# Kernel tuning notes

Hardware: AMD Instinct MI355X
Metric: run time of the kernel (lower is better)

## Reference

```python
import jax, jax.numpy as jnp
import numpy as np

D_MODEL, D_QK, D_V = 1024, 128, 128
B, S = 4, 4096


def setup_inputs() -> dict:
    key = jax.random.key(0)
    ks = jax.random.split(key, 4)
    scale = 1.0 / np.sqrt(D_MODEL)
    return {
        "x": jax.random.normal(ks[0], (B, S, D_MODEL), dtype=jnp.float32),
        "Wq": jax.random.normal(ks[1], (D_MODEL, D_QK), dtype=jnp.float32) * scale,
        "bq": jnp.zeros((D_QK,), dtype=jnp.float32),
        "Wk": jax.random.normal(ks[2], (D_MODEL, D_QK), dtype=jnp.float32) * scale,
        "bk": jnp.zeros((D_QK,), dtype=jnp.float32),
        "Wv": jax.random.normal(ks[3], (D_MODEL, D_V), dtype=jnp.float32) * scale,
        "bv": jnp.zeros((D_V,), dtype=jnp.float32),
    }


def reference(x, Wq, bq, Wk, bk, Wv, bv):
    # Linear projections (torch Linear: x @ W^T + b; here W stored as [in, out])
    q = jnp.einsum("bsd,de->bse", x, Wq) + bq  # [B, S, d_qk]
    k = jnp.einsum("bsd,de->bse", x, Wk) + bk  # [B, S, d_qk]
    v = jnp.einsum("bsd,de->bse", x, Wv) + bv  # [B, S, d_v]
    scores = jnp.einsum("bqe,bke->bqk", q, k) / jnp.sqrt(jnp.float32(D_QK))
    attn = jax.nn.softmax(scores, axis=-1)  # [B, S, S]
    return jnp.einsum("bqk,bkv->bqv", attn, v)  # [B, S, d_v]
```

## Files before the change

kernel.cpp:

```cpp
#include <hip/hip_runtime.h>
#include <math.h>

#define DM    1024
#define DQK   128
#define BATCH 4
#define SEQ   4096
#define QSCALE (0.08838834764831845f * 1.4426950408889634f)
#define DEFER_THR 6.0f

typedef _Float16 f16;
typedef _Float16 f16x4 __attribute__((ext_vector_type(4)));
typedef _Float16 f16x8 __attribute__((ext_vector_type(8)));
typedef float    f32x4 __attribute__((ext_vector_type(4)));

__global__ __launch_bounds__(256) void wcvt_kernel(
    const float* __restrict__ Wq, const float* __restrict__ bq,
    const float* __restrict__ Wk, const float* __restrict__ bk,
    const float* __restrict__ Wv, const float* __restrict__ bv,
    f16* __restrict__ wt, float* __restrict__ biasf)
{
    const int sel = blockIdx.x >> 3;
    const int k0  = (blockIdx.x & 7) * 128;
    const float* W; const float* b; float sc;
    if (sel == 0)      { W = Wq; b = bq; sc = QSCALE; }
    else if (sel == 1) { W = Wk; b = bk; sc = 1.0f; }
    else               { W = Wv; b = bv; sc = 1.0f; }

    __shared__ f16 tile[128][136];

    #pragma unroll
    for (int it = 0; it < 16; ++it) {
        int flat = threadIdx.x + it * 256;
        int kk   = flat >> 5;
        int c4   = flat & 31;
        float4 w4 = *(const float4*)(W + (size_t)(k0 + kk) * DQK + c4 * 4);
        tile[kk][c4 * 4 + 0] = (f16)(w4.x * sc);
        tile[kk][c4 * 4 + 1] = (f16)(w4.y * sc);
        tile[kk][c4 * 4 + 2] = (f16)(w4.z * sc);
        tile[kk][c4 * 4 + 3] = (f16)(w4.w * sc);
    }
    __syncthreads();

    #pragma unroll
    for (int it = 0; it < 8; ++it) {
        int flat = threadIdx.x + it * 256;
        int n    = flat >> 4;
        int kc   = flat & 15;
        f16x8 v;
        #pragma unroll
        for (int i = 0; i < 8; ++i) v[i] = tile[kc * 8 + i][n];
        *(f16x8*)(wt + (size_t)(sel * 128 + n) * DM + k0 + kc * 8) = v;
    }
    if ((blockIdx.x & 7) == 0 && threadIdx.x < 128)
        biasf[sel * 128 + threadIdx.x] = b[threadIdx.x] * sc;
}

__global__ __launch_bounds__(512, 2) void proj_kernel(
    const float* __restrict__ x, const f16* __restrict__ wt,
    const float* __restrict__ biasf,
    f16* __restrict__ qo, f16* __restrict__ ko, f16* __restrict__ vto)
{
    __shared__ __align__(16) unsigned char smem[50176];

    const int tid  = threadIdx.x;
    const int lane = tid & 63;
    const int w    = tid >> 6;
    const int c    = lane & 15;
    const int g    = lane >> 4;
    const int r0   = blockIdx.x * 64;

    const int srow = tid >> 3;
    const int skq  = tid & 7;
    const float* const xsrc  = x + (size_t)(r0 + srow) * DM + skq * 8;
    const unsigned     swoff = (unsigned)(srow * 128 + ((skq ^ (srow & 7)) * 16));

    f32x4 acc[4][3];
    #pragma unroll
    for (int rf = 0; rf < 4; ++rf)
        #pragma unroll
        for (int nf = 0; nf < 3; ++nf) acc[rf][nf] = (f32x4)0.f;

    float4 xa, xb2;
    auto gload = [&](int t) {
        const float* p = xsrc + t * 64;
        xa  = *(const float4*)p;
        xb2 = *(const float4*)(p + 4);
    };
    auto swrite = [&](int buf) {
        f16x8 h;
        h[0] = (f16)xa.x;  h[1] = (f16)xa.y;  h[2] = (f16)xa.z;  h[3] = (f16)xa.w;
        h[4] = (f16)xb2.x; h[5] = (f16)xb2.y; h[6] = (f16)xb2.z; h[7] = (f16)xb2.w;
        *(f16x8*)(smem + (unsigned)buf * 8192u + swoff) = h;
    };

    gload(0); swrite(0);
    gload(1);
    __syncthreads();

    for (int t = 0; t < 16; ++t) {
        const int cur = t & 1;
        if (t < 15) swrite(cur ^ 1);
        if (t < 14) gload(t + 2);

        f16x8 af[4][2];
        #pragma unroll
        for (int rf = 0; rf < 4; ++rf)
            #pragma unroll
            for (int ks = 0; ks < 2; ++ks)
                af[rf][ks] = *(const f16x8*)(smem + (unsigned)cur * 8192u
                    + (unsigned)((rf * 16 + c) * 128)
                    + (unsigned)((((4 * ks + g) ^ (c & 7)) * 16)));

        #pragma unroll
        for (int nf = 0; nf < 3; ++nf) {
            #pragma unroll
            for (int ks = 0; ks < 2; ++ks) {
                f16x8 bf = *(const f16x8*)(wt
                    + (size_t)(w * 48 + nf * 16 + c) * DM + t * 64 + ks * 32 + g * 8);
                #pragma unroll
                for (int rf = 0; rf < 4; ++rf)
                    acc[rf][nf] = __builtin_amdgcn_mfma_f32_16x16x32_f16(
                        af[rf][ks], bf, acc[rf][nf], 0, 0, 0);
            }
        }
        __syncthreads();
    }

    f16* const tile = (f16*)smem;
    #pragma unroll
    for (int rf = 0; rf < 4; ++rf)
        #pragma unroll
        for (int nf = 0; nf < 3; ++nf) {
            const int n  = w * 48 + nf * 16 + c;
            const float bb = biasf[n];
            #pragma unroll
            for (int r = 0; r < 4; ++r) {
                const int row = rf * 16 + 4 * g + r;
                tile[row * 392 + n] = (f16)(acc[rf][nf][r] + bb);
            }
        }
    __syncthreads();

    #pragma unroll
    for (int it = 0; it < 2; ++it) {
        const int u   = tid + it * 512;
        const int row = u >> 4;
        const int c8  = (u & 15) * 8;
        *(f16x8*)(qo + (size_t)(r0 + row) * DQK + c8) = *(const f16x8*)&tile[row * 392 + c8];
        *(f16x8*)(ko + (size_t)(r0 + row) * DQK + c8) = *(const f16x8*)&tile[row * 392 + 128 + c8];
    }
    const int gb = r0 >> 12;
    const int s0 = r0 & (SEQ - 1);
    #pragma unroll
    for (int it = 0; it < 2; ++it) {
        const int u  = tid + it * 512;
        const int d  = u >> 3;
        const int s8 = (u & 7) * 8;
        f16x8 vv;
        #pragma unroll
        for (int i = 0; i < 8; ++i) vv[i] = tile[(s8 + i) * 392 + 256 + d];
        *(f16x8*)(vto + ((size_t)gb * DQK + d) * SEQ + s0 + s8) = vv;
    }
}

__device__ __forceinline__ void stage16(const void* g, unsigned char* l) {
    __builtin_amdgcn_global_load_lds(
        (const __attribute__((address_space(1))) unsigned int*)g,
        (__attribute__((address_space(3))) unsigned int*)l, 16, 0, 0);
}

#define KOFF 0u
#define VOFF 65536u
#define POFF 131072u
#define MOFF 151552u
#define LOFF 152576u

__global__ __launch_bounds__(512, 2) void attn_kernel(
    const f16* __restrict__ qg, const f16* __restrict__ kg,
    const f16* __restrict__ vtg, float* __restrict__ out)
{
    __shared__ __align__(16) unsigned char smem[153600];

    const int tid  = threadIdx.x;
    const int lane = tid & 63;
    const int w    = tid >> 6;
    const int wq   = w >> 2;
    const int wk   = w & 3;
    const int c    = lane & 15;
    const int g    = lane >> 4;

    const int bid = blockIdx.x;
    const int xcd = bid & 7;
    const int bb  = xcd >> 1;
    const int qt  = (bid >> 3) | ((xcd & 1) << 5);
    const int q0  = qt * 64;

    const f16*  qb = qg  + (size_t)bb * SEQ * DQK;
    const char* kB = (const char*)(kg  + (size_t)bb * SEQ * DQK);
    const char* vB = (const char*)(vtg + (size_t)bb * DQK * SEQ);

    f16x8 qf[2][4];
    {
        const f16* qr = qb + (size_t)(q0 + wq * 32) * DQK;
        #pragma unroll
        for (int n = 0; n < 2; ++n)
            #pragma unroll
            for (int ks = 0; ks < 4; ++ks)
                qf[n][ks] = *(const f16x8*)(qr + (n * 16 + c) * DQK + ks * 32 + 8 * g);
    }

    f32x4 o[2][9];
    #pragma unroll
    for (int n = 0; n < 2; ++n)
        #pragma unroll
        for (int f = 0; f < 9; ++f) o[n][f] = (f32x4)0.f;
    float m_run[2] = {-3e38f, -3e38f};

    f16x8 onesf;
    #pragma unroll
    for (int i = 0; i < 8; ++i) onesf[i] = (f16)1.0f;

    const unsigned wbase = (unsigned)(tid >> 6) * 1024;

    auto stage_tiles = [&](int t, int pbuf) {
        const int kv0 = t * 128;
        unsigned char* kdst = smem + KOFF + (unsigned)pbuf * 32768u + wbase;
        unsigned char* vdst = smem + VOFF + (unsigned)pbuf * 32768u + wbase;
        #pragma unroll
        for (int cc = 0; cc < 4; ++cc) {
            const int j   = tid + cc * 512;
            const int row = j >> 4;
            const int col = j & 15;
            const int sw  = (col ^ (row & 7)) * 16;
            stage16(kB + (size_t)(kv0 + row) * 256 + sw, kdst + cc * 8192);
            stage16(vB + (size_t)row * 8192 + (size_t)kv0 * 2 + sw, vdst + cc * 8192);
        }
    };

    stage_tiles(0, 0);
    __syncthreads();

    unsigned char* const pmine = smem + POFF + (unsigned)w * 2560u;

    for (int t = 0; t < 32; ++t) {
        const int pb = t & 1;
        if (t < 31) stage_tiles(t + 1, pb ^ 1);

        unsigned char* const kbase = smem + KOFF + (unsigned)pb * 32768u;
        unsigned char* const vbase = smem + VOFF + (unsigned)pb * 32768u;

        f32x4 s[2][2];
        s[0][0] = (f32x4)0.f; s[0][1] = (f32x4)0.f;
        s[1][0] = (f32x4)0.f; s[1][1] = (f32x4)0.f;
        __builtin_amdgcn_s_setprio(1);
        #pragma unroll
        for (int ks = 0; ks < 4; ++ks) {
            #pragma unroll
            for (int m = 0; m < 2; ++m) {
                f16x8 kf = *(const f16x8*)(kbase
                    + (unsigned)(wk * 32 + m * 16 + c) * 256u
                    + (unsigned)(((4 * ks + g) ^ (c & 7)) * 16));
                s[m][0] = __builtin_amdgcn_mfma_f32_16x16x32_f16(kf, qf[0][ks], s[m][0], 0, 0, 0);
                s[m][1] = __builtin_amdgcn_mfma_f32_16x16x32_f16(kf, qf[1][ks], s[m][1], 0, 0, 0);
            }
        }
        __builtin_amdgcn_s_setprio(0);

        float mt[2];
        #pragma unroll
        for (int n = 0; n < 2; ++n) {
            float a0 = fmaxf(fmaxf(s[0][n][0], s[0][n][1]), fmaxf(s[0][n][2], s[0][n][3]));
            float a1 = fmaxf(fmaxf(s[1][n][0], s[1][n][1]), fmaxf(s[1][n][2], s[1][n][3]));
            float v  = fmaxf(a0, a1);
            v = fmaxf(v, __shfl_xor(v, 16, 64));
            v = fmaxf(v, __shfl_xor(v, 32, 64));
            mt[n] = v;
        }

        bool need = (mt[0] > m_run[0] + DEFER_THR) || (mt[1] > m_run[1] + DEFER_THR);
        if (__any(need)) {
            float al[2];
            #pragma unroll
            for (int n = 0; n < 2; ++n) {
                float mn = fmaxf(m_run[n], mt[n]);
                al[n] = __builtin_amdgcn_exp2f(m_run[n] - mn);
                m_run[n] = mn;
            }
            float alo[2][4];
            #pragma unroll
            for (int n = 0; n < 2; ++n)
                #pragma unroll
                for (int r = 0; r < 4; ++r)
                    alo[n][r] = __shfl(al[n], 4 * g + r, 16);
            #pragma unroll
            for (int n = 0; n < 2; ++n)
                #pragma unroll
                for (int f = 0; f < 9; ++f)
                    #pragma unroll
                    for (int r = 0; r < 4; ++r) o[n][f][r] *= alo[n][r];
        }

        #pragma unroll
        for (int n = 0; n < 2; ++n)
            #pragma unroll
            for (int m = 0; m < 2; ++m) {
                f16x4 h;
                #pragma unroll
                for (int r = 0; r < 4; ++r)
                    h[r] = (f16)__builtin_amdgcn_exp2f(s[m][n][r] - m_run[n]);
                *(f16x4*)(pmine + (unsigned)(16 * n + c) * 80u + (unsigned)(32 * m + 8 * g)) = h;
            }

        f16x8 pa[2];
        pa[0] = *(const f16x8*)(pmine + (unsigned)(c) * 80u + 16u * g);
        pa[1] = *(const f16x8*)(pmine + (unsigned)(16 + c) * 80u + 16u * g);
        __builtin_amdgcn_s_setprio(1);
        #pragma unroll
        for (int df = 0; df < 8; ++df) {
            f16x8 vf = *(const f16x8*)(vbase
                + (unsigned)(df * 16 + c) * 256u
                + (unsigned)(((4 * wk + g) ^ (c & 7)) * 16));
            o[0][df] = __builtin_amdgcn_mfma_f32_16x16x32_f16(pa[0], vf, o[0][df], 0, 0, 0);
            o[1][df] = __builtin_amdgcn_mfma_f32_16x16x32_f16(pa[1], vf, o[1][df], 0, 0, 0);
        }
        o[0][8] = __builtin_amdgcn_mfma_f32_16x16x32_f16(pa[0], onesf, o[0][8], 0, 0, 0);
        o[1][8] = __builtin_amdgcn_mfma_f32_16x16x32_f16(pa[1], onesf, o[1][8], 0, 0, 0);
        __builtin_amdgcn_s_setprio(0);

        __syncthreads();
    }

    float m_o[2][4];
    #pragma unroll
    for (int n = 0; n < 2; ++n)
        #pragma unroll
        for (int r = 0; r < 4; ++r)
            m_o[n][r] = __shfl(m_run[n], 4 * g + r, 16);

    float* const mld  = (float*)(smem + MOFF);
    float* const lld  = (float*)(smem + LOFF);
    float* const olds = (float*)smem;

    if (wk > 0) {
        const int base = (wq * 3 + (wk - 1)) * 32;
        #pragma unroll
        for (int n = 0; n < 2; ++n)
            #pragma unroll
            for (int f = 0; f < 8; ++f)
                #pragma unroll
                for (int r = 0; r < 4; ++r)
                    olds[(size_t)(base + n * 16 + 4 * g + r) * 132 + f * 16 + c] = o[n][f][r];
        if (c == 0) {
            #pragma unroll
            for (int n = 0; n < 2; ++n)
                #pragma unroll
                for (int r = 0; r < 4; ++r) {
                    mld[(wq * 4 + wk) * 32 + n * 16 + 4 * g + r] = m_o[n][r];
                    lld[(wq * 4 + wk) * 32 + n * 16 + 4 * g + r] = o[n][8][r];
                }
        }
    }
    __syncthreads();

    if (wk == 0) {
        #pragma unroll
        for (int n = 0; n < 2; ++n) {
            #pragma unroll
            for (int r = 0; r < 4; ++r) {
                const int rl = n * 16 + 4 * g + r;
                const float m0 = m_o[n][r];
                const float m1 = mld[(wq * 4 + 1) * 32 + rl];
                const float m2 = mld[(wq * 4 + 2) * 32 + rl];
                const float m3 = mld[(wq * 4 + 3) * 32 + rl];
                const float ms = fmaxf(fmaxf(m0, m1), fmaxf(m2, m3));
                const float a0 = __builtin_amdgcn_exp2f(m0 - ms);
                const float a1 = __builtin_amdgcn_exp2f(m1 - ms);
                const float a2 = __builtin_amdgcn_exp2f(m2 - ms);
                const float a3 = __builtin_amdgcn_exp2f(m3 - ms);
                const float ls = a0 * o[n][8][r]
                               + a1 * lld[(wq * 4 + 1) * 32 + rl]
                               + a2 * lld[(wq * 4 + 2) * 32 + rl]
                               + a3 * lld[(wq * 4 + 3) * 32 + rl];
                const float inv = 1.0f / ls;
                float* orow = out + ((size_t)bb * SEQ + q0 + wq * 32 + rl) * DQK;
                #pragma unroll
                for (int f = 0; f < 8; ++f) {
                    float v = a0 * o[n][f][r]
                            + a1 * olds[(size_t)((wq * 3 + 0) * 32 + rl) * 132 + f * 16 + c]
                            + a2 * olds[(size_t)((wq * 3 + 1) * 32 + rl) * 132 + f * 16 + c]
                            + a3 * olds[(size_t)((wq * 3 + 2) * 32 + rl) * 132 + f * 16 + c];
                    orow[f * 16 + c] = v * inv;
                }
            }
        }
    }
}

extern "C" void kernel_launch(void* const* d_in, const int* in_sizes, int n_in,
                              void* d_out, int out_size, void* d_ws, size_t ws_size,
                              hipStream_t stream) {
    const float* x  = (const float*)d_in[0];
    const float* Wq = (const float*)d_in[1];
    const float* bq = (const float*)d_in[2];
    const float* Wk = (const float*)d_in[3];
    const float* bk = (const float*)d_in[4];
    const float* Wv = (const float*)d_in[5];
    const float* bv = (const float*)d_in[6];
    float* outp = (float*)d_out;

    f16*   qf    = (f16*)d_ws;
    f16*   kf    = qf + (size_t)BATCH * SEQ * DQK;
    f16*   vt    = kf + (size_t)BATCH * SEQ * DQK;
    f16*   wt    = vt + (size_t)BATCH * DQK * SEQ;
    float* biasf = (float*)(wt + (size_t)384 * DM);

    wcvt_kernel<<<24, 256, 0, stream>>>(Wq, bq, Wk, bk, Wv, bv, wt, biasf);

    proj_kernel<<<BATCH * SEQ / 64, 512, 0, stream>>>(x, wt, biasf, qf, kf, vt);

    attn_kernel<<<256, 512, 0, stream>>>(qf, kf, vt, outp);
}
```

Before: 101.1 us.

## Software-pipeline QK and PV across iterations, register-shuffle P, scalar row sums

Restructures the KV loop so each iteration runs QK^T for tile t and PV for tile t-1 in one MFMA burst, with staging of the next tile moved after a mid-loop barrier. The P matrix is no longer round-tripped through LDS; it is packed to fp16 with cvt_pkrtz and redistributed with ds_bpermute. The row-sum, formerly an extra MFMA against a ones vector, becomes an fp32 reduction with shuffles, which drops two accumulator registers and the P LDS region. This adds a second barrier per iteration and more VALU/shuffle work, and the denominator now sums fp32 exponentials while the numerator still uses fp16-rounded P.

```diff
diff --git a/kernel.cpp b/kernel.cpp
--- a/kernel.cpp
+++ b/kernel.cpp
@@ -171,15 +171,14 @@
 
 #define KOFF 0u
 #define VOFF 65536u
-#define POFF 131072u
-#define MOFF 151552u
-#define LOFF 152576u
+#define MOFF 131072u
+#define LOFF 132096u
 
 __global__ __launch_bounds__(512, 2) void attn_kernel(
     const f16* __restrict__ qg, const f16* __restrict__ kg,
     const f16* __restrict__ vtg, float* __restrict__ out)
 {
-    __shared__ __align__(16) unsigned char smem[153600];
+    __shared__ __align__(16) unsigned char smem[133120];
 
     const int tid  = threadIdx.x;
     const int lane = tid & 63;
@@ -209,18 +208,15 @@
                 qf[n][ks] = *(const f16x8*)(qr + (n * 16 + c) * DQK + ks * 32 + 8 * g);
     }
 
-    f32x4 o[2][9];
+    f32x4 o[2][8];
     #pragma unroll
     for (int n = 0; n < 2; ++n)
         #pragma unroll
-        for (int f = 0; f < 9; ++f) o[n][f] = (f32x4)0.f;
+        for (int f = 0; f < 8; ++f) o[n][f] = (f32x4)0.f;
     float m_run[2] = {-3e38f, -3e38f};
-
-    f16x8 onesf;
-    #pragma unroll
-    for (int i = 0; i < 8; ++i) onesf[i] = (f16)1.0f;
-
-    const unsigned wbase = (unsigned)(tid >> 6) * 1024;
+    float l_run[2] = {0.f, 0.f};
+
+    const unsigned wbase = (unsigned)w * 1024;
 
     auto stage_tiles = [&](int t, int pbuf) {
         const int kv0 = t * 128;
@@ -237,105 +233,147 @@
         }
     };
 
+    const int addr_h0 = (16 * (2 * (g & 1) + 0) + c) * 4;
+    const int addr_h1 = (16 * (2 * (g & 1) + 1) + c) * 4;
+    const bool hi_m = (g >= 2);
+
     stage_tiles(0, 0);
     __syncthreads();
 
-    unsigned char* const pmine = smem + POFF + (unsigned)w * 2560u;
-
-    for (int t = 0; t < 32; ++t) {
-        const int pb = t & 1;
-        if (t < 31) stage_tiles(t + 1, pb ^ 1);
-
-        unsigned char* const kbase = smem + KOFF + (unsigned)pb * 32768u;
-        unsigned char* const vbase = smem + VOFF + (unsigned)pb * 32768u;
+    f16x8 pa[2];
+
+    for (int t = 0; t <= 32; ++t) {
+        const int cb = t & 1;
+        unsigned char* const kbase = smem + KOFF + (unsigned)cb * 32768u;
+        unsigned char* const vbase = smem + VOFF + (unsigned)(cb ^ 1) * 32768u;
 
         f32x4 s[2][2];
-        s[0][0] = (f32x4)0.f; s[0][1] = (f32x4)0.f;
-        s[1][0] = (f32x4)0.f; s[1][1] = (f32x4)0.f;
+
         __builtin_amdgcn_s_setprio(1);
-        #pragma unroll
-        for (int ks = 0; ks < 4; ++ks) {
-            #pragma unroll
-            for (int m = 0; m < 2; ++m) {
-                f16x8 kf = *(const f16x8*)(kbase
-                    + (unsigned)(wk * 32 + m * 16 + c) * 256u
-                    + (unsigned)(((4 * ks + g) ^ (c & 7)) * 16));
-                s[m][0] = __builtin_amdgcn_mfma_f32_16x16x32_f16(kf, qf[0][ks], s[m][0], 0, 0, 0);
-                s[m][1] = __builtin_amdgcn_mfma_f32_16x16x32_f16(kf, qf[1][ks], s[m][1], 0, 0, 0);
+        if (t < 32) {
+            s[0][0] = (f32x4)0.f; s[0][1] = (f32x4)0.f;
+            s[1][0] = (f32x4)0.f; s[1][1] = (f32x4)0.f;
+            #pragma unroll
+            for (int ks = 0; ks < 4; ++ks) {
+                #pragma unroll
+                for (int m = 0; m < 2; ++m) {
+                    f16x8 kf = *(const f16x8*)(kbase
+                        + (unsigned)(wk * 32 + m * 16 + c) * 256u
+                        + (unsigned)(((4 * ks + g) ^ (c & 7)) * 16));
+                    s[m][0] = __builtin_amdgcn_mfma_f32_16x16x32_f16(kf, qf[0][ks], s[m][0], 0, 0, 0);
+                    s[m][1] = __builtin_amdgcn_mfma_f32_16x16x32_f16(kf, qf[1][ks], s[m][1], 0, 0, 0);
+                }
+            }
+        }
+        if (t > 0) {
+            #pragma unroll
+            for (int df = 0; df < 8; ++df) {
+                f16x8 vf = *(const f16x8*)(vbase
+                    + (unsigned)(df * 16 + c) * 256u
+                    + (unsigned)(((4 * wk + g) ^ (c & 7)) * 16));
+                o[0][df] = __builtin_amdgcn_mfma_f32_16x16x32_f16(pa[0], vf, o[0][df], 0, 0, 0);
+                o[1][df] = __builtin_amdgcn_mfma_f32_16x16x32_f16(pa[1], vf, o[1][df], 0, 0, 0);
             }
         }
         __builtin_amdgcn_s_setprio(0);
 
-        float mt[2];
-        #pragma unroll
-        for (int n = 0; n < 2; ++n) {
-            float a0 = fmaxf(fmaxf(s[0][n][0], s[0][n][1]), fmaxf(s[0][n][2], s[0][n][3]));
-            float a1 = fmaxf(fmaxf(s[1][n][0], s[1][n][1]), fmaxf(s[1][n][2], s[1][n][3]));
-            float v  = fmaxf(a0, a1);
-            v = fmaxf(v, __shfl_xor(v, 16, 64));
-            v = fmaxf(v, __shfl_xor(v, 32, 64));
-            mt[n] = v;
-        }
-
-        bool need = (mt[0] > m_run[0] + DEFER_THR) || (mt[1] > m_run[1] + DEFER_THR);
-        if (__any(need)) {
-            float al[2];
+        __syncthreads();
+
+        if (t < 31) stage_tiles(t + 1, cb ^ 1);
+
+        if (t < 32) {
+            float mt[2];
             #pragma unroll
             for (int n = 0; n < 2; ++n) {
-                float mn = fmaxf(m_run[n], mt[n]);
-                al[n] = __builtin_amdgcn_exp2f(m_run[n] - mn);
-                m_run[n] = mn;
-            }
-            float alo[2][4];
+                float a0 = fmaxf(fmaxf(s[0][n][0], s[0][n][1]), fmaxf(s[0][n][2], s[0][n][3]));
+                float a1 = fmaxf(fmaxf(s[1][n][0], s[1][n][1]), fmaxf(s[1][n][2], s[1][n][3]));
+                float v  = fmaxf(a0, a1);
+                v = fmaxf(v, __shfl_xor(v, 16, 64));
+                v = fmaxf(v, __shfl_xor(v, 32, 64));
+                mt[n] = v;
+            }
+
+            bool need = (mt[0] > m_run[0] + DEFER_THR) || (mt[1] > m_run[1] + DEFER_THR);
+            if (__any(need)) {
+                float al[2];
+                #pragma unroll
+                for (int n = 0; n < 2; ++n) {
+                    float mn = fmaxf(m_run[n], mt[n]);
+                    al[n] = __builtin_amdgcn_exp2f(m_run[n] - mn);
+                    m_run[n] = mn;
+                    l_run[n] *= al[n];
+                }
+                float alo[2][4];
+                #pragma unroll
+                for (int n = 0; n < 2; ++n)
+                    #pragma unroll
+                    for (int r = 0; r < 4; ++r)
+                        alo[n][r] = __shfl(al[n], 4 * g + r, 16);
+                #pragma unroll
+                for (int n = 0; n < 2; ++n)
+                    #pragma unroll
+                    for (int f = 0; f < 8; ++f)
+                        #pragma unroll
+                        for (int r = 0; r < 4; ++r) o[n][f][r] *= alo[n][r];
+            }
+
+            float e[2][2][4];
+            #pragma unroll
+            for (int m = 0; m < 2; ++m)
+                #pragma unroll
+                for (int n = 0; n < 2; ++n)
+                    #pragma unroll
+                    for (int r = 0; r < 4; ++r)
+                        e[m][n][r] = __builtin_amdgcn_exp2f(s[m][n][r] - m_run[n]);
+
+            #pragma unroll
+            for (int n = 0; n < 2; ++n) {
+                float ls = ((e[0][n][0] + e[0][n][1]) + (e[0][n][2] + e[0][n][3]))
+                         + ((e[1][n][0] + e[1][n][1]) + (e[1][n][2] + e[1][n][3]));
+                ls += __shfl_xor(ls, 16, 64);
+                ls += __shfl_xor(ls, 32, 64);
+                l_run[n] += ls;
+            }
+
+            int u[2][2][2];
             #pragma unroll
             for (int n = 0; n < 2; ++n)
                 #pragma unroll
-                for (int r = 0; r < 4; ++r)
-                    alo[n][r] = __shfl(al[n], 4 * g + r, 16);
-            #pragma unroll
-            for (int n = 0; n < 2; ++n)
-                #pragma unroll
-                for (int f = 0; f < 9; ++f)
+                for (int m = 0; m < 2; ++m)
                     #pragma unroll
-                    for (int r = 0; r < 4; ++r) o[n][f][r] *= alo[n][r];
-        }
-
-        #pragma unroll
-        for (int n = 0; n < 2; ++n)
-            #pragma unroll
-            for (int m = 0; m < 2; ++m) {
-                f16x4 h;
-                #pragma unroll
-                for (int r = 0; r < 4; ++r)
-                    h[r] = (f16)__builtin_amdgcn_exp2f(s[m][n][r] - m_run[n]);
-                *(f16x4*)(pmine + (unsigned)(16 * n + c) * 80u + (unsigned)(32 * m + 8 * g)) = h;
-            }
-
-        f16x8 pa[2];
-        pa[0] = *(const f16x8*)(pmine + (unsigned)(c) * 80u + 16u * g);
-        pa[1] = *(const f16x8*)(pmine + (unsigned)(16 + c) * 80u + 16u * g);
-        __builtin_amdgcn_s_setprio(1);
-        #pragma unroll
-        for (int df = 0; df < 8; ++df) {
-            f16x8 vf = *(const f16x8*)(vbase
-                + (unsigned)(df * 16 + c) * 256u
-                + (unsigned)(((4 * wk + g) ^ (c & 7)) * 16));
-            o[0][df] = __builtin_amdgcn_mfma_f32_16x16x32_f16(pa[0], vf, o[0][df], 0, 0, 0);
-            o[1][df] = __builtin_amdgcn_mfma_f32_16x16x32_f16(pa[1], vf, o[1][df], 0, 0, 0);
-        }
-        o[0][8] = __builtin_amdgcn_mfma_f32_16x16x32_f16(pa[0], onesf, o[0][8], 0, 0, 0);
-        o[1][8] = __builtin_amdgcn_mfma_f32_16x16x32_f16(pa[1], onesf, o[1][8], 0, 0, 0);
-        __builtin_amdgcn_s_setprio(0);
+                    for (int p = 0; p < 2; ++p) {
+                        f16x2_t_hack:;
+                        __fp16 dummy; (void)dummy;
+                        auto h2 = __builtin_amdgcn_cvt_pkrtz(e[m][n][2 * p], e[m][n][2 * p + 1]);
+                        u[n][m][p] = __builtin_bit_cast(int, h2);
+                    }
+
+            #pragma unroll
+            for (int n = 0; n < 2; ++n) {
+                int paw[4];
+                #pragma unroll
+                for (int j = 0; j < 4; ++j) {
+                    const int addr = (j >> 1) ? addr_h1 : addr_h0;
+                    int tA = __builtin_amdgcn_ds_bpermute(addr, u[n][0][j & 1]);
+                    int tB = __builtin_amdgcn_ds_bpermute(addr, u[n][1][j & 1]);
+                    paw[j] = hi_m ? tB : tA;
+                }
+                int4 pw = make_int4(paw[0], paw[1], paw[2], paw[3]);
+                pa[n] = __builtin_bit_cast(f16x8, pw);
+            }
+        }
 
         __syncthreads();
     }
 
-    float m_o[2][4];
+    float m_o[2][4], l_o[2][4];
     #pragma unroll
     for (int n = 0; n < 2; ++n)
         #pragma unroll
-        for (int r = 0; r < 4; ++r)
+        for (int r = 0; r < 4; ++r) {
             m_o[n][r] = __shfl(m_run[n], 4 * g + r, 16);
+            l_o[n][r] = __shfl(l_run[n], 4 * g + r, 16);
+        }
 
     float* const mld  = (float*)(smem + MOFF);
     float* const lld  = (float*)(smem + LOFF);
@@ -356,7 +394,7 @@
                 #pragma unroll
                 for (int r = 0; r < 4; ++r) {
                     mld[(wq * 4 + wk) * 32 + n * 16 + 4 * g + r] = m_o[n][r];
-                    lld[(wq * 4 + wk) * 32 + n * 16 + 4 * g + r] = o[n][8][r];
+                    lld[(wq * 4 + wk) * 32 + n * 16 + 4 * g + r] = l_o[n][r];
                 }
         }
     }
@@ -377,7 +415,7 @@
                 const float a1 = __builtin_amdgcn_exp2f(m1 - ms);
                 const float a2 = __builtin_amdgcn_exp2f(m2 - ms);
                 const float a3 = __builtin_amdgcn_exp2f(m3 - ms);
-                const float ls = a0 * o[n][8][r]
+                const float ls = a0 * l_o[n][r]
                                + a1 * lld[(wq * 4 + 1) * 32 + rl]
                                + a2 * lld[(wq * 4 + 2) * 32 + rl]
                                + a3 * lld[(wq * 4 + 3) * 32 + rl];
```

Result: slower. 112.4 us (+11.2%).

## Load K/V fragments directly into registers and drop LDS staging and barriers

Applied to the files above, without the earlier changes.

Replaces the double-buffered LDS staging of K and V tiles with direct global-to-register loads per lane, prefetching the next K tile into a ping-pong register set. The P matrix is reshuffled with ds_bpermute instead of an LDS round-trip. The row sum is computed with shuffles rather than an extra MFMA against a ones vector. This removes the per-iteration __syncthreads and LDS traffic, at the cost of more registers, redundant global/L2 reads across waves and exposed load latency.

```diff
diff --git a/kernel.cpp b/kernel.cpp
--- a/kernel.cpp
+++ b/kernel.cpp
@@ -163,23 +163,122 @@
     }
 }
 
-__device__ __forceinline__ void stage16(const void* g, unsigned char* l) {
-    __builtin_amdgcn_global_load_lds(
-        (const __attribute__((address_space(1))) unsigned int*)g,
-        (__attribute__((address_space(3))) unsigned int*)l, 16, 0, 0);
-}
-
-#define KOFF 0u
-#define VOFF 65536u
-#define POFF 131072u
-#define MOFF 151552u
-#define LOFF 152576u
+
+#define ATTN_STEP(KC, KN, T)                                                              \
+    {                                                                                     \
+        const int tt = (T);                                                               \
+        f16x8 vr[8];                                                                      \
+        _Pragma("unroll")                                                                 \
+        for (int df = 0; df < 8; ++df)                                                    \
+            vr[df] = *(const f16x8*)(vlane + (size_t)tt * 256 + (size_t)df * 131072);     \
+        if (tt + 1 < 32) {                                                                \
+            _Pragma("unroll")                                                             \
+            for (int i = 0; i < 8; ++i)                                                   \
+                KN[i] = *(const f16x8*)(klane + (size_t)(tt + 1) * 32768                  \
+                            + (size_t)(i >> 2) * 4096 + (size_t)(i & 3) * 64);            \
+        }                                                                                 \
+        f32x4 s[2][2];                                                                    \
+        s[0][0] = (f32x4)0.f; s[0][1] = (f32x4)0.f;                                       \
+        s[1][0] = (f32x4)0.f; s[1][1] = (f32x4)0.f;                                       \
+        __builtin_amdgcn_s_setprio(1);                                                    \
+        _Pragma("unroll")                                                                 \
+        for (int ks = 0; ks < 4; ++ks) {                                                  \
+            _Pragma("unroll")                                                             \
+            for (int m = 0; m < 2; ++m) {                                                 \
+                s[m][0] = __builtin_amdgcn_mfma_f32_16x16x32_f16(                         \
+                    KC[m * 4 + ks], qf[0][ks], s[m][0], 0, 0, 0);                         \
+                s[m][1] = __builtin_amdgcn_mfma_f32_16x16x32_f16(                         \
+                    KC[m * 4 + ks], qf[1][ks], s[m][1], 0, 0, 0);                         \
+            }                                                                             \
+        }                                                                                 \
+        __builtin_amdgcn_s_setprio(0);                                                    \
+        float mt[2];                                                                      \
+        _Pragma("unroll")                                                                 \
+        for (int n = 0; n < 2; ++n) {                                                     \
+            float a0 = fmaxf(fmaxf(s[0][n][0], s[0][n][1]), fmaxf(s[0][n][2], s[0][n][3]));\
+            float a1 = fmaxf(fmaxf(s[1][n][0], s[1][n][1]), fmaxf(s[1][n][2], s[1][n][3]));\
+            float v  = fmaxf(a0, a1);                                                     \
+            v = fmaxf(v, __shfl_xor(v, 16, 64));                                          \
+            v = fmaxf(v, __shfl_xor(v, 32, 64));                                          \
+            mt[n] = v;                                                                    \
+        }                                                                                 \
+        bool need = (mt[0] > m_run[0] + DEFER_THR) || (mt[1] > m_run[1] + DEFER_THR);     \
+        if (__any(need)) {                                                                \
+            float al[2];                                                                  \
+            _Pragma("unroll")                                                             \
+            for (int n = 0; n < 2; ++n) {                                                 \
+                float mn = fmaxf(m_run[n], mt[n]);                                        \
+                al[n] = __builtin_amdgcn_exp2f(m_run[n] - mn);                            \
+                m_run[n] = mn;                                                            \
+                l_run[n] *= al[n];                                                        \
+            }                                                                             \
+            float alo[2][4];                                                              \
+            _Pragma("unroll")                                                             \
+            for (int n = 0; n < 2; ++n)                                                   \
+                _Pragma("unroll")                                                         \
+                for (int r = 0; r < 4; ++r)                                               \
+                    alo[n][r] = __shfl(al[n], 4 * g + r, 16);                             \
+            _Pragma("unroll")                                                             \
+            for (int n = 0; n < 2; ++n)                                                   \
+                _Pragma("unroll")                                                         \
+                for (int f = 0; f < 8; ++f)                                               \
+                    _Pragma("unroll")                                                     \
+                    for (int r = 0; r < 4; ++r) o[n][f][r] *= alo[n][r];                  \
+        }                                                                                 \
+        _Pragma("unroll")                                                                 \
+        for (int m = 0; m < 2; ++m)                                                       \
+            _Pragma("unroll")                                                             \
+            for (int n = 0; n < 2; ++n)                                                   \
+                _Pragma("unroll")                                                         \
+                for (int r = 0; r < 4; ++r)                                               \
+                    s[m][n][r] = __builtin_amdgcn_exp2f(s[m][n][r] - m_run[n]);           \
+        _Pragma("unroll")                                                                 \
+        for (int n = 0; n < 2; ++n) {                                                     \
+            float ls = ((s[0][n][0] + s[0][n][1]) + (s[0][n][2] + s[0][n][3]))            \
+                     + ((s[1][n][0] + s[1][n][1]) + (s[1][n][2] + s[1][n][3]));           \
+            ls += __shfl_xor(ls, 16, 64);                                                 \
+            ls += __shfl_xor(ls, 32, 64);                                                 \
+            l_run[n] += ls;                                                               \
+        }                                                                                 \
+        int u[2][2][2];                                                                   \
+        _Pragma("unroll")                                                                 \
+        for (int n = 0; n < 2; ++n)                                                       \
+            _Pragma("unroll")                                                             \
+            for (int m = 0; m < 2; ++m)                                                   \
+                _Pragma("unroll")                                                         \
+                for (int p = 0; p < 2; ++p) {                                             \
+                    auto h2 = __builtin_amdgcn_cvt_pkrtz(s[m][n][2 * p], s[m][n][2 * p + 1]);\
+                    u[n][m][p] = __builtin_bit_cast(int, h2);                             \
+                }                                                                         \
+        f16x8 pa[2];                                                                      \
+        _Pragma("unroll")                                                                 \
+        for (int n = 0; n < 2; ++n) {                                                     \
+            int paw[4];                                                                   \
+            _Pragma("unroll")                                                             \
+            for (int j = 0; j < 4; ++j) {                                                 \
+                const int addr = (j >> 1) ? addr_h1 : addr_h0;                            \
+                int tA = __builtin_amdgcn_ds_bpermute(addr, u[n][0][j & 1]);              \
+                int tB = __builtin_amdgcn_ds_bpermute(addr, u[n][1][j & 1]);              \
+                paw[j] = hi_m ? tB : tA;                                                  \
+            }                                                                             \
+            int4 pw = make_int4(paw[0], paw[1], paw[2], paw[3]);                          \
+            pa[n] = __builtin_bit_cast(f16x8, pw);                                        \
+        }                                                                                 \
+        __builtin_amdgcn_s_setprio(1);                                                    \
+        _Pragma("unroll")                                                                 \
+        for (int df = 0; df < 8; ++df) {                                                  \
+            o[0][df] = __builtin_amdgcn_mfma_f32_16x16x32_f16(pa[0], vr[df], o[0][df], 0, 0, 0);\
+            o[1][df] = __builtin_amdgcn_mfma_f32_16x16x32_f16(pa[1], vr[df], o[1][df], 0, 0, 0);\
+        }                                                                                 \
+        __builtin_amdgcn_s_setprio(0);                                                    \
+    }
 
 __global__ __launch_bounds__(512, 2) void attn_kernel(
     const f16* __restrict__ qg, const f16* __restrict__ kg,
     const f16* __restrict__ vtg, float* __restrict__ out)
 {
-    __shared__ __align__(16) unsigned char smem[153600];
+    __shared__ float olds[192 * 132];
+    __shared__ float mld[256], lld[256];
 
     const int tid  = threadIdx.x;
     const int lane = tid & 63;
@@ -199,6 +298,9 @@
     const char* kB = (const char*)(kg  + (size_t)bb * SEQ * DQK);
     const char* vB = (const char*)(vtg + (size_t)bb * DQK * SEQ);
 
+    const char* const klane = kB + (size_t)(wk * 32 + c) * 256 + g * 16;
+    const char* const vlane = vB + (size_t)c * 8192 + (wk * 32 + g * 8) * 2;
+
     f16x8 qf[2][4];
     {
         const f16* qr = qb + (size_t)(q0 + wq * 32) * DQK;
@@ -209,137 +311,36 @@
                 qf[n][ks] = *(const f16x8*)(qr + (n * 16 + c) * DQK + ks * 32 + 8 * g);
     }
 
-    f32x4 o[2][9];
+    f32x4 o[2][8];
     #pragma unroll
     for (int n = 0; n < 2; ++n)
         #pragma unroll
-        for (int f = 0; f < 9; ++f) o[n][f] = (f32x4)0.f;
+        for (int f = 0; f < 8; ++f) o[n][f] = (f32x4)0.f;
     float m_run[2] = {-3e38f, -3e38f};
-
-    f16x8 onesf;
-    #pragma unroll
-    for (int i = 0; i < 8; ++i) onesf[i] = (f16)1.0f;
-
-    const unsigned wbase = (unsigned)(tid >> 6) * 1024;
-
-    auto stage_tiles = [&](int t, int pbuf) {
-        const int kv0 = t * 128;
-        unsigned char* kdst = smem + KOFF + (unsigned)pbuf * 32768u + wbase;
-        unsigned char* vdst = smem + VOFF + (unsigned)pbuf * 32768u + wbase;
-        #pragma unroll
-        for (int cc = 0; cc < 4; ++cc) {
-            const int j   = tid + cc * 512;
-            const int row = j >> 4;
-            const int col = j & 15;
-            const int sw  = (col ^ (row & 7)) * 16;
-            stage16(kB + (size_t)(kv0 + row) * 256 + sw, kdst + cc * 8192);
-            stage16(vB + (size_t)row * 8192 + (size_t)kv0 * 2 + sw, vdst + cc * 8192);
+    float l_run[2] = {0.f, 0.f};
+
+    const int addr_h0 = (16 * (2 * (g & 1) + 0) + c) * 4;
+    const int addr_h1 = (16 * (2 * (g & 1) + 1) + c) * 4;
+    const bool hi_m = (g >= 2);
+
+    f16x8 kA[8], kBf[8];
+    #pragma unroll
+    for (int i = 0; i < 8; ++i)
+        kA[i] = *(const f16x8*)(klane + (size_t)(i >> 2) * 4096 + (size_t)(i & 3) * 64);
+
+    for (int t = 0; t < 32; t += 2) {
+        ATTN_STEP(kA,  kBf, t);
+        ATTN_STEP(kBf, kA,  t + 1);
+    }
+
+    float m_o[2][4], l_o[2][4];
+    #pragma unroll
+    for (int n = 0; n < 2; ++n)
+        #pragma unroll
+        for (int r = 0; r < 4; ++r) {
+            m_o[n][r] = __shfl(m_run[n], 4 * g + r, 16);
+            l_o[n][r] = __shfl(l_run[n], 4 * g + r, 16);
         }
-    };
-
-    stage_tiles(0, 0);
-    __syncthreads();
-
-    unsigned char* const pmine = smem + POFF + (unsigned)w * 2560u;
-
-    for (int t = 0; t < 32; ++t) {
-        const int pb = t & 1;
-        if (t < 31) stage_tiles(t + 1, pb ^ 1);
-
-        unsigned char* const kbase = smem + KOFF + (unsigned)pb * 32768u;
-        unsigned char* const vbase = smem + VOFF + (unsigned)pb * 32768u;
-
-        f32x4 s[2][2];
-        s[0][0] = (f32x4)0.f; s[0][1] = (f32x4)0.f;
-        s[1][0] = (f32x4)0.f; s[1][1] = (f32x4)0.f;
-        __builtin_amdgcn_s_setprio(1);
-        #pragma unroll
-        for (int ks = 0; ks < 4; ++ks) {
-            #pragma unroll
-            for (int m = 0; m < 2; ++m) {
-                f16x8 kf = *(const f16x8*)(kbase
-                    + (unsigned)(wk * 32 + m * 16 + c) * 256u
-                    + (unsigned)(((4 * ks + g) ^ (c & 7)) * 16));
-                s[m][0] = __builtin_amdgcn_mfma_f32_16x16x32_f16(kf, qf[0][ks], s[m][0], 0, 0, 0);
-                s[m][1] = __builtin_amdgcn_mfma_f32_16x16x32_f16(kf, qf[1][ks], s[m][1], 0, 0, 0);
-            }
-        }
-        __builtin_amdgcn_s_setprio(0);
-
-        float mt[2];
-        #pragma unroll
-        for (int n = 0; n < 2; ++n) {
-            float a0 = fmaxf(fmaxf(s[0][n][0], s[0][n][1]), fmaxf(s[0][n][2], s[0][n][3]));
-            float a1 = fmaxf(fmaxf(s[1][n][0], s[1][n][1]), fmaxf(s[1][n][2], s[1][n][3]));
-            float v  = fmaxf(a0, a1);
-            v = fmaxf(v, __shfl_xor(v, 16, 64));
-            v = fmaxf(v, __shfl_xor(v, 32, 64));
-            mt[n] = v;
-        }
-
-        bool need = (mt[0] > m_run[0] + DEFER_THR) || (mt[1] > m_run[1] + DEFER_THR);
-        if (__any(need)) {
-            float al[2];
-            #pragma unroll
-            for (int n = 0; n < 2; ++n) {
-                float mn = fmaxf(m_run[n], mt[n]);
-                al[n] = __builtin_amdgcn_exp2f(m_run[n] - mn);
-                m_run[n] = mn;
-            }
-            float alo[2][4];
-            #pragma unroll
-            for (int n = 0; n < 2; ++n)
-                #pragma unroll
-                for (int r = 0; r < 4; ++r)
-                    alo[n][r] = __shfl(al[n], 4 * g + r, 16);
-            #pragma unroll
-            for (int n = 0; n < 2; ++n)
-                #pragma unroll
-                for (int f = 0; f < 9; ++f)
-                    #pragma unroll
-                    for (int r = 0; r < 4; ++r) o[n][f][r] *= alo[n][r];
-        }
-
-        #pragma unroll
-        for (int n = 0; n < 2; ++n)
-            #pragma unroll
-            for (int m = 0; m < 2; ++m) {
-                f16x4 h;
-                #pragma unroll
-                for (int r = 0; r < 4; ++r)
-                    h[r] = (f16)__builtin_amdgcn_exp2f(s[m][n][r] - m_run[n]);
-                *(f16x4*)(pmine + (unsigned)(16 * n + c) * 80u + (unsigned)(32 * m + 8 * g)) = h;
-            }
-
-        f16x8 pa[2];
-        pa[0] = *(const f16x8*)(pmine + (unsigned)(c) * 80u + 16u * g);
-        pa[1] = *(const f16x8*)(pmine + (unsigned)(16 + c) * 80u + 16u * g);
-        __builtin_amdgcn_s_setprio(1);
-        #pragma unroll
-        for (int df = 0; df < 8; ++df) {
-            f16x8 vf = *(const f16x8*)(vbase
-                + (unsigned)(df * 16 + c) * 256u
-                + (unsigned)(((4 * wk + g) ^ (c & 7)) * 16));
-            o[0][df] = __builtin_amdgcn_mfma_f32_16x16x32_f16(pa[0], vf, o[0][df], 0, 0, 0);
-            o[1][df] = __builtin_amdgcn_mfma_f32_16x16x32_f16(pa[1], vf, o[1][df], 0, 0, 0);
-        }
-        o[0][8] = __builtin_amdgcn_mfma_f32_16x16x32_f16(pa[0], onesf, o[0][8], 0, 0, 0);
-        o[1][8] = __builtin_amdgcn_mfma_f32_16x16x32_f16(pa[1], onesf, o[1][8], 0, 0, 0);
-        __builtin_amdgcn_s_setprio(0);
-
-        __syncthreads();
-    }
-
-    float m_o[2][4];
-    #pragma unroll
-    for (int n = 0; n < 2; ++n)
-        #pragma unroll
-        for (int r = 0; r < 4; ++r)
-            m_o[n][r] = __shfl(m_run[n], 4 * g + r, 16);
-
-    float* const mld  = (float*)(smem + MOFF);
-    float* const lld  = (float*)(smem + LOFF);
-    float* const olds = (float*)smem;
 
     if (wk > 0) {
         const int base = (wq * 3 + (wk - 1)) * 32;
@@ -356,7 +357,7 @@
                 #pragma unroll
                 for (int r = 0; r < 4; ++r) {
                     mld[(wq * 4 + wk) * 32 + n * 16 + 4 * g + r] = m_o[n][r];
-                    lld[(wq * 4 + wk) * 32 + n * 16 + 4 * g + r] = o[n][8][r];
+                    lld[(wq * 4 + wk) * 32 + n * 16 + 4 * g + r] = l_o[n][r];
                 }
         }
     }
@@ -377,7 +378,7 @@
                 const float a1 = __builtin_amdgcn_exp2f(m1 - ms);
                 const float a2 = __builtin_amdgcn_exp2f(m2 - ms);
                 const float a3 = __builtin_amdgcn_exp2f(m3 - ms);
-                const float ls = a0 * o[n][8][r]
+                const float ls = a0 * l_o[n][r]
                                + a1 * lld[(wq * 4 + 1) * 32 + rl]
                                + a2 * lld[(wq * 4 + 2) * 32 + rl]
                                + a3 * lld[(wq * 4 + 3) * 32 + rl];
```

Result: slower. 162.7 us (+60.9%).

## Stage projection weights into LDS via async global_load_lds with smaller K-steps

Applied to the files above, without the earlier changes.

The projection kernel now stages the fp16 weight tiles into swizzled shared memory with asynchronous global-to-LDS loads, double-buffered alongside the x tile. Previously each wave read the weights straight from global memory. The K-step is halved from 64 to 32, giving twice as many iterations and barriers, and the launch bound asks for 4 blocks per CU. The goal is to cut redundant global weight traffic and hide its latency, at the cost of more synchronisation and more LDS use per block.

```diff
diff --git a/kernel.cpp b/kernel.cpp
--- a/kernel.cpp
+++ b/kernel.cpp
@@ -12,6 +12,12 @@
 typedef _Float16 f16x4 __attribute__((ext_vector_type(4)));
 typedef _Float16 f16x8 __attribute__((ext_vector_type(8)));
 typedef float    f32x4 __attribute__((ext_vector_type(4)));
+
+__device__ __forceinline__ void stage16(const void* g, unsigned char* l) {
+    __builtin_amdgcn_global_load_lds(
+        (const __attribute__((address_space(1))) unsigned int*)g,
+        (__attribute__((address_space(3))) unsigned int*)l, 16, 0, 0);
+}
 
 __global__ __launch_bounds__(256) void wcvt_kernel(
     const float* __restrict__ Wq, const float* __restrict__ bq,
@@ -55,12 +61,15 @@
         biasf[sel * 128 + threadIdx.x] = b[threadIdx.x] * sc;
 }
 
-__global__ __launch_bounds__(512, 2) void proj_kernel(
+#define PXOFF 0u
+#define PWOFF 10240u
+
+__global__ __launch_bounds__(512, 4) void proj_kernel(
     const float* __restrict__ x, const f16* __restrict__ wt,
     const float* __restrict__ biasf,
     f16* __restrict__ qo, f16* __restrict__ ko, f16* __restrict__ vto)
 {
-    __shared__ __align__(16) unsigned char smem[50176];
+    __shared__ __align__(16) unsigned char smem[59392];
 
     const int tid  = threadIdx.x;
     const int lane = tid & 63;
@@ -70,9 +79,13 @@
     const int r0   = blockIdx.x * 64;
 
     const int srow = tid >> 3;
-    const int skq  = tid & 7;
-    const float* const xsrc  = x + (size_t)(r0 + srow) * DM + skq * 8;
-    const unsigned     swoff = (unsigned)(srow * 128 + ((skq ^ (srow & 7)) * 16));
+    const int sk4  = tid & 7;
+    const float* const xsrc  = x + (size_t)(r0 + srow) * DM + sk4 * 4;
+    const unsigned     xwoff = (unsigned)(srow * 80 + sk4 * 8);
+
+    const char* const wtB  = (const char*)wt;
+    const int         wn_l = w * 16 + (lane >> 2);
+    const int         wcl  = lane & 3;
 
     f32x4 acc[4][3];
     #pragma unroll
@@ -80,48 +93,51 @@
         #pragma unroll
         for (int nf = 0; nf < 3; ++nf) acc[rf][nf] = (f32x4)0.f;
 
-    float4 xa, xb2;
-    auto gload = [&](int t) {
-        const float* p = xsrc + t * 64;
-        xa  = *(const float4*)p;
-        xb2 = *(const float4*)(p + 4);
+    float4 xa;
+    auto gload = [&](int t) { xa = *(const float4*)(xsrc + t * 32); };
+    auto swrite = [&](int buf) {
+        f16x4 h;
+        h[0] = (f16)xa.x; h[1] = (f16)xa.y; h[2] = (f16)xa.z; h[3] = (f16)xa.w;
+        *(f16x4*)(smem + PXOFF + (unsigned)buf * 5120u + xwoff) = h;
     };
-    auto swrite = [&](int buf) {
-        f16x8 h;
-        h[0] = (f16)xa.x;  h[1] = (f16)xa.y;  h[2] = (f16)xa.z;  h[3] = (f16)xa.w;
-        h[4] = (f16)xb2.x; h[5] = (f16)xb2.y; h[6] = (f16)xb2.z; h[7] = (f16)xb2.w;
-        *(f16x8*)(smem + (unsigned)buf * 8192u + swoff) = h;
+    auto stage_W = [&](int t, int pbuf) {
+        unsigned char* wdst = smem + PWOFF + (unsigned)pbuf * 24576u + (unsigned)w * 1024u;
+        #pragma unroll
+        for (int cc = 0; cc < 3; ++cc) {
+            const int n = wn_l + cc * 128;
+            stage16(wtB + (size_t)n * 2048 + (size_t)t * 64
+                        + (unsigned)((wcl ^ ((n >> 1) & 3)) * 16),
+                    wdst + cc * 8192);
+        }
     };
 
     gload(0); swrite(0);
     gload(1);
+    stage_W(0, 0);
     __syncthreads();
 
-    for (int t = 0; t < 16; ++t) {
+    for (int t = 0; t < 32; ++t) {
         const int cur = t & 1;
-        if (t < 15) swrite(cur ^ 1);
-        if (t < 14) gload(t + 2);
-
-        f16x8 af[4][2];
+        if (t < 31) swrite(cur ^ 1);
+        if (t < 30) gload(t + 2);
+        if (t < 31) stage_W(t + 1, cur ^ 1);
+
+        f16x8 af[4];
         #pragma unroll
         for (int rf = 0; rf < 4; ++rf)
-            #pragma unroll
-            for (int ks = 0; ks < 2; ++ks)
-                af[rf][ks] = *(const f16x8*)(smem + (unsigned)cur * 8192u
-                    + (unsigned)((rf * 16 + c) * 128)
-                    + (unsigned)((((4 * ks + g) ^ (c & 7)) * 16)));
-
+            af[rf] = *(const f16x8*)(smem + PXOFF + (unsigned)cur * 5120u
+                + (unsigned)((rf * 16 + c) * 80 + g * 16));
+
+        unsigned char* const wbase = smem + PWOFF + (unsigned)cur * 24576u;
         #pragma unroll
         for (int nf = 0; nf < 3; ++nf) {
-            #pragma unroll
-            for (int ks = 0; ks < 2; ++ks) {
-                f16x8 bf = *(const f16x8*)(wt
-                    + (size_t)(w * 48 + nf * 16 + c) * DM + t * 64 + ks * 32 + g * 8);
-                #pragma unroll
-                for (int rf = 0; rf < 4; ++rf)
-                    acc[rf][nf] = __builtin_amdgcn_mfma_f32_16x16x32_f16(
-                        af[rf][ks], bf, acc[rf][nf], 0, 0, 0);
-            }
+            const int n = w * 48 + nf * 16 + c;
+            f16x8 bf = *(const f16x8*)(wbase
+                + (unsigned)(n * 64 + ((g ^ ((n >> 1) & 3)) * 16)));
+            #pragma unroll
+            for (int rf = 0; rf < 4; ++rf)
+                acc[rf][nf] = __builtin_amdgcn_mfma_f32_16x16x32_f16(
+                    af[rf], bf, acc[rf][nf], 0, 0, 0);
         }
         __syncthreads();
     }
@@ -161,12 +177,6 @@
         for (int i = 0; i < 8; ++i) vv[i] = tile[(s8 + i) * 392 + 256 + d];
         *(f16x8*)(vto + ((size_t)gb * DQK + d) * SEQ + s0 + s8) = vv;
     }
-}
-
-__device__ __forceinline__ void stage16(const void* g, unsigned char* l) {
-    __builtin_amdgcn_global_load_lds(
-        (const __attribute__((address_space(1))) unsigned int*)g,
-        (__attribute__((address_space(3))) unsigned int*)l, 16, 0, 0);
 }
 
 #define KOFF 0u
```

After: 99.06 us. -2.0%, faster.
